# Optimization experiments

Hardware: AMD Instinct MI355X
Metric: run time of the kernel (lower is better)

Reference implementation:

```python
import jax, jax.numpy as jnp
import numpy as np

EMBED = 1024
HEADS = 16
HEAD_DIM = EMBED // HEADS


def setup_inputs() -> dict:
    key = jax.random.key(0)
    k1, k2, k3 = jax.random.split(key, 3)
    hidden_states = jax.random.normal(k1, (2, 2048, EMBED), dtype=jnp.float32)
    # Conv1D weights are stored (nx, nf): y = x @ W + b
    c_attn_w = jax.random.normal(k2, (EMBED, 3 * EMBED), dtype=jnp.float32) * 0.02
    c_attn_b = jnp.zeros((3 * EMBED,), dtype=jnp.float32)
    c_proj_w = jax.random.normal(k3, (EMBED, EMBED), dtype=jnp.float32) * 0.02
    c_proj_b = jnp.zeros((EMBED,), dtype=jnp.float32)
    return {
        "hidden_states": hidden_states,
        "c_attn_w": c_attn_w,
        "c_attn_b": c_attn_b,
        "c_proj_w": c_proj_w,
        "c_proj_b": c_proj_b,
    }


def reference(hidden_states, c_attn_w, c_attn_b, c_proj_w, c_proj_b):
    B, S, E = hidden_states.shape
    H, D = HEADS, HEAD_DIM
    fused = hidden_states @ c_attn_w + c_attn_b  # [B,S,3E]
    q, k, v = jnp.split(fused, 3, axis=-1)
    # split heads -> [B,H,S,D]
    q = q.reshape(B, S, H, D).transpose(0, 2, 1, 3)
    k = k.reshape(B, S, H, D).transpose(0, 2, 1, 3)
    v = v.reshape(B, S, H, D).transpose(0, 2, 1, 3)
    scores = jnp.einsum("bhqd,bhkd->bhqk", q, k) / jnp.sqrt(jnp.float32(D))
    probs = jax.nn.softmax(scores, axis=-1)  # NOTE: no causal mask in source
    attn = jnp.einsum("bhqk,bhkd->bhqd", probs, v)
    out = attn.transpose(0, 2, 1, 3).reshape(B, S, E)
    return out @ c_proj_w + c_proj_b
```

## Files before the change

### kernel.cpp

```cpp
#include <hip/hip_runtime.h>
#include <hip/hip_bf16.h>
#include <cstdint>
#include <cstddef>

#define E_ 1024
#define H_ 16
#define D_ 64
#define B_ 2
#define S_ 2048
#define T_ 4096
#define NQ_ 3072

typedef __bf16 bf16_t;
typedef bf16_t bf16x8 __attribute__((ext_vector_type(8)));
typedef float f32x4 __attribute__((ext_vector_type(4)));

static __device__ __forceinline__ unsigned short f2bf(float f) {
    __hip_bfloat16 h = __float2bfloat16(f);
    return __builtin_bit_cast(unsigned short, h);
}
static __device__ __forceinline__ unsigned pack2(float a, float b) {
    return (unsigned)f2bf(a) | ((unsigned)f2bf(b) << 16);
}
static __device__ __forceinline__ unsigned cvt_pk(float a, float b) {
    unsigned r;
    asm("v_cvt_pk_bf16_f32 %0, %1, %2" : "=v"(r) : "v"(a), "v"(b));
    return r;
}
static __device__ __forceinline__ bf16x8 ld_frag(const unsigned short* p) {
    uint4 u = *reinterpret_cast<const uint4*>(p);
    return __builtin_bit_cast(bf16x8, u);
}
static __device__ __forceinline__ void cp16(unsigned short* lds, const unsigned short* g) {
    __builtin_amdgcn_global_load_lds(
        (const __attribute__((address_space(1))) unsigned int*)g,
        (__attribute__((address_space(3))) unsigned int*)lds, 16, 0, 0);
}
static __device__ __forceinline__ f32x4 mfma16(bf16x8 a, bf16x8 b, f32x4 c) {
    return __builtin_amdgcn_mfma_f32_16x16x32_bf16(a, b, c, 0, 0, 0);
}

__global__ __launch_bounds__(256) void k_cvt(const float* __restrict__ in,
                                             unsigned short* __restrict__ out, int n) {
    int i = (blockIdx.x * 256 + threadIdx.x) * 4;
    if (i < n) {
        float4 v = *reinterpret_cast<const float4*>(in + i);
        uint2 o;
        o.x = pack2(v.x, v.y);
        o.y = pack2(v.z, v.w);
        *reinterpret_cast<uint2*>(out + i) = o;
    }
}

__global__ __launch_bounds__(256) void k_wt(const float* __restrict__ in,
                                            unsigned short* __restrict__ out, int K, int N) {
    __shared__ float t[32][33];
    int n0 = blockIdx.x * 32, k0 = blockIdx.y * 32;
    int tx = threadIdx.x, ty = threadIdx.y;
    for (int j = 0; j < 4; j++) {
        int r = ty + j * 8;
        t[r][tx] = in[(size_t)(k0 + r) * N + n0 + tx];
    }
    __syncthreads();
    for (int j = 0; j < 4; j++) {
        int r = ty + j * 8;
        out[(size_t)(n0 + r) * K + k0 + tx] = f2bf(t[tx][r]);
    }
}

static __device__ __forceinline__ void gemm_tile_128(
    const unsigned short* __restrict__ A,
    const unsigned short* __restrict__ Bt,
    int Ktot, int m0, int n0,
    unsigned short* As, unsigned short* Bs,
    f32x4 acc[4][4])
{
    const int t = threadIdx.x;
    const int w = t >> 6, lane = t & 63, lr = lane & 15, lq = lane >> 4;
    const int wm = (w >> 1) * 64, wn = (w & 1) * 64;
    for (int mt = 0; mt < 4; mt++)
        for (int nt = 0; nt < 4; nt++)
            acc[mt][nt] = (f32x4){0.f, 0.f, 0.f, 0.f};

    for (int kt = 0; kt < Ktot; kt += 32) {
        __syncthreads();
        for (int i = 0; i < 2; i++) {
            int c = t + i * 256;
            int row = c >> 2, kp = (c & 3) * 8;
            cp16(&As[c * 8], &A[(size_t)(m0 + row) * Ktot + kt + kp]);
        }
        for (int i = 0; i < 2; i++) {
            int c = t + i * 256;
            int row = c >> 2, kp = (c & 3) * 8;
            cp16(&Bs[c * 8], &Bt[(size_t)(n0 + row) * Ktot + kt + kp]);
        }
        __syncthreads();
        bf16x8 af[4], bfr[4];
        for (int mt = 0; mt < 4; mt++) af[mt]  = ld_frag(&As[(wm + mt * 16 + lr) * 32 + lq * 8]);
        for (int nt = 0; nt < 4; nt++) bfr[nt] = ld_frag(&Bs[(wn + nt * 16 + lr) * 32 + lq * 8]);
        for (int mt = 0; mt < 4; mt++)
            for (int nt = 0; nt < 4; nt++)
                acc[mt][nt] = mfma16(af[mt], bfr[nt], acc[mt][nt]);
    }
}

__global__ __launch_bounds__(256) void k_qkv(
    const unsigned short* __restrict__ Ab, const unsigned short* __restrict__ Wt,
    const float* __restrict__ bias,
    unsigned short* __restrict__ Qb, unsigned short* __restrict__ Kb,
    unsigned short* __restrict__ Vb)
{
    __shared__ __attribute__((aligned(16))) unsigned short As[128 * 32];
    __shared__ __attribute__((aligned(16))) unsigned short Bs[128 * 32];
    f32x4 acc[4][4];
    int m0 = blockIdx.x * 128, n0 = blockIdx.y * 128;
    gemm_tile_128(Ab, Wt, E_, m0, n0, As, Bs, acc);

    int t = threadIdx.x, w = t >> 6, lane = t & 63, lr = lane & 15, lq = lane >> 4;
    int wm = (w >> 1) * 64, wn = (w & 1) * 64;
    int sector = (n0 >> 10);
    for (int nt = 0; nt < 4; nt++) {
        int n = n0 + wn + nt * 16 + lr;
        float bv = bias[n];
        int nn = n & 1023, h = nn >> 6, d = nn & 63;
        for (int mt = 0; mt < 4; mt++) {
            for (int i = 0; i < 4; i++) {
                int tok = m0 + wm + mt * 16 + lq * 4 + i;
                int b = tok >> 11, s = tok & 2047;
                float v = acc[mt][nt][i] + bv;
                if (sector == 0) {
                    Qb[(((size_t)(b * H_ + h) * S_ + s) << 6) + d] = f2bf(v * 0.18033688f);
                } else if (sector == 1) {
                    Kb[(((size_t)(b * H_ + h) * S_ + s) << 6) + d] = f2bf(v);
                } else {
                    Vb[(((size_t)(b * H_ + h) * D_ + d) << 11) + s] = f2bf(v);
                }
            }
        }
    }
}

__global__ __launch_bounds__(256) void k_attn(
    const unsigned short* __restrict__ Qb, const unsigned short* __restrict__ Kb,
    const unsigned short* __restrict__ Vb, unsigned short* __restrict__ Ob)
{
    __shared__ __attribute__((aligned(16))) unsigned short Ks[2][128 * 64];
    __shared__ __attribute__((aligned(16))) unsigned short Vt[2][64 * 128];
    __shared__ __attribute__((aligned(16))) unsigned short Ps[4][32 * 64];

    const int t = threadIdx.x, w = t >> 6, lane = t & 63, lr = lane & 15, lq = lane >> 4;
    const int h = blockIdx.y, b = blockIdx.z;
    const size_t head = ((size_t)(b * H_ + h)) * (S_ * D_);
    const unsigned short* Qh = Qb + head;
    const unsigned short* Kh = Kb + head;
    const unsigned short* Vh = Vb + head;
    const int q0 = blockIdx.x * 128 + w * 16;
    const int swz = lr & 7;

    bf16x8 qa[2][2];
    for (int qh = 0; qh < 2; qh++)
        for (int kk = 0; kk < 2; kk++)
            qa[qh][kk] = ld_frag(&Qh[(size_t)(q0 + qh * 64 + lr) * 64 + kk * 32 + lq * 8]);

    f32x4 o[2][4];
    for (int qh = 0; qh < 2; qh++)
        for (int i = 0; i < 4; i++) o[qh][i] = (f32x4){0.f, 0.f, 0.f, 0.f};
    float lsum[2] = {0.f, 0.f};
    unsigned short* Pw = Ps[w];

    auto stage = [&](int bb, int kt) {
        for (int i = 0; i < 4; i++) {
            int c = t + i * 256;
            int row = c >> 3, sp = c & 7;
            cp16(&Ks[bb][c * 8], &Kh[(size_t)(kt + row) * 64 + (sp ^ (row & 7)) * 8]);
        }
        for (int i = 0; i < 4; i++) {
            int c = t + i * 256;
            int d = c >> 4, sp = c & 15, seg = (sp & 8) | ((sp & 7) ^ (d & 7));
            cp16(&Vt[bb][c * 8], &Vh[(size_t)d * S_ + kt + seg * 8]);
        }
    };

    stage(0, 0);
    asm volatile("s_waitcnt vmcnt(0)" ::: "memory");
    __syncthreads();

    int cur = 0;
#pragma unroll 2
    for (int kt = 0; kt < S_; kt += 128) {
        if (kt + 128 < S_) stage(cur ^ 1, kt + 128);

        const unsigned short* Kc = Ks[cur];
        const unsigned short* Vc = Vt[cur];

#pragma unroll
        for (int ss = 0; ss < 2; ss++) {
            for (int tau = 0; tau < 4; tau++) {
                int krow = ss * 64 + tau * 16 + lr;
                bf16x8 kf0 = ld_frag(&Kc[krow * 64 + ((0 + lq) ^ swz) * 8]);
                bf16x8 kf1 = ld_frag(&Kc[krow * 64 + ((4 + lq) ^ swz) * 8]);
                for (int qh = 0; qh < 2; qh++) {
                    f32x4 z = (f32x4){0.f, 0.f, 0.f, 0.f};
                    __builtin_amdgcn_s_setprio(1);
                    z = mfma16(kf0, qa[qh][0], z);
                    z = mfma16(kf1, qa[qh][1], z);
                    __builtin_amdgcn_s_setprio(0);
                    float e0 = __builtin_amdgcn_exp2f(z[0]);
                    float e1 = __builtin_amdgcn_exp2f(z[1]);
                    float e2 = __builtin_amdgcn_exp2f(z[2]);
                    float e3 = __builtin_amdgcn_exp2f(z[3]);
                    lsum[qh] += (e0 + e1) + (e2 + e3);
                    uint2 pk;
                    pk.x = cvt_pk(e0, e1);
                    pk.y = cvt_pk(e2, e3);
                    int seg = (tau * 2 + (lq >> 1)) ^ swz;
                    *reinterpret_cast<uint2*>(&Pw[(qh * 16 + lr) * 64 + seg * 8 + (lq & 1) * 4]) = pk;
                }
            }
            for (int kk = 0; kk < 2; kk++) {
                bf16x8 pf0 = ld_frag(&Pw[(lr) * 64 + ((kk * 4 + lq) ^ swz) * 8]);
                bf16x8 pf1 = ld_frag(&Pw[(16 + lr) * 64 + ((kk * 4 + lq) ^ swz) * 8]);
                __builtin_amdgcn_s_setprio(1);
                for (int t2 = 0; t2 < 4; t2++) {
                    int vrow = t2 * 16 + lr;
                    bf16x8 vf = ld_frag(&Vc[vrow * 128 + ((ss * 8) | ((kk * 4 + lq) ^ swz)) * 8]);
                    o[0][t2] = mfma16(vf, pf0, o[0][t2]);
                    o[1][t2] = mfma16(vf, pf1, o[1][t2]);
                }
                __builtin_amdgcn_s_setprio(0);
            }
        }

        asm volatile("s_waitcnt vmcnt(0)" ::: "memory");
        __syncthreads();
        cur ^= 1;
    }

    for (int qh = 0; qh < 2; qh++) {
        float ls = lsum[qh];
        ls += __shfl_xor(ls, 16, 64);
        ls += __shfl_xor(ls, 32, 64);
        float inv = 1.0f / ls;

        int s = q0 + qh * 64 + lr;
        size_t rowoff = ((size_t)(b * S_ + s)) * E_ + h * 64;
        for (int t2 = 0; t2 < 4; t2++) {
            uint2 pk;
            pk.x = cvt_pk(o[qh][t2][0] * inv, o[qh][t2][1] * inv);
            pk.y = cvt_pk(o[qh][t2][2] * inv, o[qh][t2][3] * inv);
            *reinterpret_cast<uint2*>(&Ob[rowoff + t2 * 16 + lq * 4]) = pk;
        }
    }
}

__global__ __launch_bounds__(256) void k_proj(
    const unsigned short* __restrict__ Ab, const unsigned short* __restrict__ Wt,
    const float* __restrict__ bias, float* __restrict__ out)
{
    __shared__ __attribute__((aligned(16))) unsigned short As[128 * 32];
    __shared__ __attribute__((aligned(16))) unsigned short Bs[64 * 32];
    const int t = threadIdx.x;
    const int w = t >> 6, lane = t & 63, lr = lane & 15, lq = lane >> 4;
    const int wm = (w >> 1) * 64, wn = (w & 1) * 32;
    const int m0 = blockIdx.x * 128, n0 = blockIdx.y * 64;

    f32x4 acc[4][2];
    for (int mt = 0; mt < 4; mt++)
        for (int nt = 0; nt < 2; nt++)
            acc[mt][nt] = (f32x4){0.f, 0.f, 0.f, 0.f};

    for (int kt = 0; kt < E_; kt += 32) {
        __syncthreads();
        for (int i = 0; i < 2; i++) {
            int c = t + i * 256;
            int row = c >> 2, kp = (c & 3) * 8;
            cp16(&As[c * 8], &Ab[(size_t)(m0 + row) * E_ + kt + kp]);
        }
        {
            int c = t;
            int row = c >> 2, kp = (c & 3) * 8;
            cp16(&Bs[c * 8], &Wt[(size_t)(n0 + row) * E_ + kt + kp]);
        }
        __syncthreads();
        bf16x8 af[4], bfr[2];
        for (int mt = 0; mt < 4; mt++) af[mt]  = ld_frag(&As[(wm + mt * 16 + lr) * 32 + lq * 8]);
        for (int nt = 0; nt < 2; nt++) bfr[nt] = ld_frag(&Bs[(wn + nt * 16 + lr) * 32 + lq * 8]);
        for (int mt = 0; mt < 4; mt++)
            for (int nt = 0; nt < 2; nt++)
                acc[mt][nt] = mfma16(af[mt], bfr[nt], acc[mt][nt]);
    }

    for (int nt = 0; nt < 2; nt++) {
        int n = n0 + wn + nt * 16 + lr;
        float bv = bias[n];
        for (int mt = 0; mt < 4; mt++)
            for (int i = 0; i < 4; i++) {
                int tok = m0 + wm + mt * 16 + lq * 4 + i;
                out[(size_t)tok * E_ + n] = acc[mt][nt][i] + bv;
            }
    }
}

extern "C" void kernel_launch(void* const* d_in, const int* in_sizes, int n_in,
                              void* d_out, int out_size, void* d_ws, size_t ws_size,
                              hipStream_t stream) {
    const float* hs = (const float*)d_in[0];
    const float* w1 = (const float*)d_in[1];
    const float* b1 = (const float*)d_in[2];
    const float* w2 = (const float*)d_in[3];
    const float* b2 = (const float*)d_in[4];
    float* out = (float*)d_out;

    char* ws = (char*)d_ws;
    unsigned short* hb  = (unsigned short*)(ws);
    unsigned short* w1t = (unsigned short*)(ws + (size_t)( 8 << 20));
    unsigned short* w2t = (unsigned short*)(ws + (size_t)(14 << 20));
    unsigned short* Qb  = (unsigned short*)(ws + (size_t)(16 << 20));
    unsigned short* Kb  = (unsigned short*)(ws + (size_t)(24 << 20));
    unsigned short* Vb  = (unsigned short*)(ws + (size_t)(32 << 20));
    unsigned short* Ao  = (unsigned short*)(ws + (size_t)(40 << 20));

    k_cvt<<<dim3(T_ * E_ / 1024), dim3(256), 0, stream>>>(hs, hb, T_ * E_);
    k_wt<<<dim3(NQ_ / 32, E_ / 32), dim3(32, 8), 0, stream>>>(w1, w1t, E_, NQ_);
    k_wt<<<dim3(E_ / 32, E_ / 32), dim3(32, 8), 0, stream>>>(w2, w2t, E_, E_);
    k_qkv<<<dim3(T_ / 128, NQ_ / 128), dim3(256), 0, stream>>>(hb, w1t, b1, Qb, Kb, Vb);
    k_attn<<<dim3(S_ / 128, H_, B_), dim3(256), 0, stream>>>(Qb, Kb, Vb, Ao);
    k_proj<<<dim3(T_ / 128, E_ / 64), dim3(256), 0, stream>>>(Ao, w2t, b2, out);
}
```

Baseline: 190.9 us.

## Double-buffer GEMM tiles in QKV and proj kernels, stage V transpose via LDS

Both the QKV and output-projection GEMMs now double-buffer their LDS tiles, issuing the next k-tile's global-to-LDS copies before computing on the current one, with one barrier per iteration instead of two. MFMA sections are wrapped in s_setprio to favour the math waves. The V output, stored transposed, is first staged in LDS so each thread writes contiguous 16-byte chunks instead of scattered 2-byte stores. This costs more shared memory per block, which may lower occupancy.

```diff
diff --git a/kernel.cpp b/kernel.cpp
--- a/kernel.cpp
+++ b/kernel.cpp
@@ -68,74 +68,105 @@
     }
 }
 
-static __device__ __forceinline__ void gemm_tile_128(
-    const unsigned short* __restrict__ A,
-    const unsigned short* __restrict__ Bt,
-    int Ktot, int m0, int n0,
-    unsigned short* As, unsigned short* Bs,
-    f32x4 acc[4][4])
-{
-    const int t = threadIdx.x;
-    const int w = t >> 6, lane = t & 63, lr = lane & 15, lq = lane >> 4;
-    const int wm = (w >> 1) * 64, wn = (w & 1) * 64;
-    for (int mt = 0; mt < 4; mt++)
-        for (int nt = 0; nt < 4; nt++)
-            acc[mt][nt] = (f32x4){0.f, 0.f, 0.f, 0.f};
-
-    for (int kt = 0; kt < Ktot; kt += 32) {
-        __syncthreads();
-        for (int i = 0; i < 2; i++) {
-            int c = t + i * 256;
-            int row = c >> 2, kp = (c & 3) * 8;
-            cp16(&As[c * 8], &A[(size_t)(m0 + row) * Ktot + kt + kp]);
-        }
-        for (int i = 0; i < 2; i++) {
-            int c = t + i * 256;
-            int row = c >> 2, kp = (c & 3) * 8;
-            cp16(&Bs[c * 8], &Bt[(size_t)(n0 + row) * Ktot + kt + kp]);
-        }
-        __syncthreads();
-        bf16x8 af[4], bfr[4];
-        for (int mt = 0; mt < 4; mt++) af[mt]  = ld_frag(&As[(wm + mt * 16 + lr) * 32 + lq * 8]);
-        for (int nt = 0; nt < 4; nt++) bfr[nt] = ld_frag(&Bs[(wn + nt * 16 + lr) * 32 + lq * 8]);
-        for (int mt = 0; mt < 4; mt++)
-            for (int nt = 0; nt < 4; nt++)
-                acc[mt][nt] = mfma16(af[mt], bfr[nt], acc[mt][nt]);
-    }
-}
-
 __global__ __launch_bounds__(256) void k_qkv(
     const unsigned short* __restrict__ Ab, const unsigned short* __restrict__ Wt,
     const float* __restrict__ bias,
     unsigned short* __restrict__ Qb, unsigned short* __restrict__ Kb,
     unsigned short* __restrict__ Vb)
 {
-    __shared__ __attribute__((aligned(16))) unsigned short As[128 * 32];
-    __shared__ __attribute__((aligned(16))) unsigned short Bs[128 * 32];
+    __shared__ __attribute__((aligned(16))) unsigned short smem[16896];
+    unsigned short* As = smem;
+    unsigned short* Bs = smem + 8192;
+
+    const int t = threadIdx.x;
+    const int w = t >> 6, lane = t & 63, lr = lane & 15, lq = lane >> 4;
+    const int wm = (w >> 1) * 64, wn = (w & 1) * 64;
+    const int m0 = blockIdx.x * 128, n0 = blockIdx.y * 128;
+
     f32x4 acc[4][4];
-    int m0 = blockIdx.x * 128, n0 = blockIdx.y * 128;
-    gemm_tile_128(Ab, Wt, E_, m0, n0, As, Bs, acc);
-
-    int t = threadIdx.x, w = t >> 6, lane = t & 63, lr = lane & 15, lq = lane >> 4;
-    int wm = (w >> 1) * 64, wn = (w & 1) * 64;
-    int sector = (n0 >> 10);
-    for (int nt = 0; nt < 4; nt++) {
-        int n = n0 + wn + nt * 16 + lr;
-        float bv = bias[n];
-        int nn = n & 1023, h = nn >> 6, d = nn & 63;
-        for (int mt = 0; mt < 4; mt++) {
-            for (int i = 0; i < 4; i++) {
-                int tok = m0 + wm + mt * 16 + lq * 4 + i;
-                int b = tok >> 11, s = tok & 2047;
-                float v = acc[mt][nt][i] + bv;
-                if (sector == 0) {
-                    Qb[(((size_t)(b * H_ + h) * S_ + s) << 6) + d] = f2bf(v * 0.18033688f);
-                } else if (sector == 1) {
-                    Kb[(((size_t)(b * H_ + h) * S_ + s) << 6) + d] = f2bf(v);
-                } else {
-                    Vb[(((size_t)(b * H_ + h) * D_ + d) << 11) + s] = f2bf(v);
+    for (int mt = 0; mt < 4; mt++)
+        for (int nt = 0; nt < 4; nt++)
+            acc[mt][nt] = (f32x4){0.f, 0.f, 0.f, 0.f};
+
+    auto stage = [&](int bb, int kt) {
+        for (int i = 0; i < 2; i++) {
+            int c = t + i * 256;
+            int row = c >> 2, kp = (c & 3) * 8;
+            cp16(&As[bb * 4096 + c * 8], &Ab[(size_t)(m0 + row) * E_ + kt + kp]);
+        }
+        for (int i = 0; i < 2; i++) {
+            int c = t + i * 256;
+            int row = c >> 2, kp = (c & 3) * 8;
+            cp16(&Bs[bb * 4096 + c * 8], &Wt[(size_t)(n0 + row) * E_ + kt + kp]);
+        }
+    };
+
+    stage(0, 0);
+    asm volatile("s_waitcnt vmcnt(0)" ::: "memory");
+    __syncthreads();
+
+    int cur = 0;
+    for (int kt = 0; kt < E_; kt += 32) {
+        if (kt + 32 < E_) stage(cur ^ 1, kt + 32);
+        const unsigned short* Ac = &As[cur * 4096];
+        const unsigned short* Bc = &Bs[cur * 4096];
+        bf16x8 af[4], bfr[4];
+        for (int mt = 0; mt < 4; mt++) af[mt]  = ld_frag(&Ac[(wm + mt * 16 + lr) * 32 + lq * 8]);
+        for (int nt = 0; nt < 4; nt++) bfr[nt] = ld_frag(&Bc[(wn + nt * 16 + lr) * 32 + lq * 8]);
+        __builtin_amdgcn_s_setprio(1);
+        for (int mt = 0; mt < 4; mt++)
+            for (int nt = 0; nt < 4; nt++)
+                acc[mt][nt] = mfma16(af[mt], bfr[nt], acc[mt][nt]);
+        __builtin_amdgcn_s_setprio(0);
+        asm volatile("s_waitcnt vmcnt(0)" ::: "memory");
+        __syncthreads();
+        cur ^= 1;
+    }
+
+    const int sector = (n0 >> 10);
+    if (sector != 2) {
+        for (int nt = 0; nt < 4; nt++) {
+            int n = n0 + wn + nt * 16 + lr;
+            float bv = bias[n];
+            int nn = n & 1023, h = nn >> 6, d = nn & 63;
+            for (int mt = 0; mt < 4; mt++) {
+                for (int i = 0; i < 4; i++) {
+                    int tok = m0 + wm + mt * 16 + lq * 4 + i;
+                    int b = tok >> 11, s = tok & 2047;
+                    float v = acc[mt][nt][i] + bv;
+                    if (sector == 0) {
+                        Qb[(((size_t)(b * H_ + h) * S_ + s) << 6) + d] = f2bf(v * 0.18033688f);
+                    } else {
+                        Kb[(((size_t)(b * H_ + h) * S_ + s) << 6) + d] = f2bf(v);
+                    }
                 }
             }
+        }
+    } else {
+        for (int nt = 0; nt < 4; nt++) {
+            int nl = wn + nt * 16 + lr;
+            int row = nl;
+            float bv = bias[n0 + nl];
+            unsigned short* vr = &smem[row * 132];
+            for (int mt = 0; mt < 4; mt++) {
+                int tokb = wm + mt * 16 + lq * 4;
+                uint2 pk;
+                pk.x = cvt_pk(acc[mt][nt][0] + bv, acc[mt][nt][1] + bv);
+                pk.y = cvt_pk(acc[mt][nt][2] + bv, acc[mt][nt][3] + bv);
+                *reinterpret_cast<uint2*>(&vr[tokb]) = pk;
+            }
+        }
+        __syncthreads();
+        int row = t >> 1, half = t & 1;
+        int hglob = ((n0 & 1023) >> 6) + (row >> 6), d = row & 63;
+        int b = m0 >> 11, sbase = (m0 & 2047) + half * 64;
+        size_t gb = (((size_t)(b * H_ + hglob) * D_ + d) << 11) + sbase;
+        const unsigned short* src = &smem[row * 132 + half * 64];
+        for (int jj = 0; jj < 8; jj++) {
+            uint2 a = *reinterpret_cast<const uint2*>(&src[jj * 8]);
+            uint2 bq = *reinterpret_cast<const uint2*>(&src[jj * 8 + 4]);
+            uint4 o4; o4.x = a.x; o4.y = a.y; o4.z = bq.x; o4.w = bq.y;
+            *reinterpret_cast<uint4*>(&Vb[gb + jj * 8]) = o4;
         }
     }
 }
@@ -257,8 +288,10 @@
     const unsigned short* __restrict__ Ab, const unsigned short* __restrict__ Wt,
     const float* __restrict__ bias, float* __restrict__ out)
 {
-    __shared__ __attribute__((aligned(16))) unsigned short As[128 * 32];
-    __shared__ __attribute__((aligned(16))) unsigned short Bs[64 * 32];
+    __shared__ __attribute__((aligned(16))) unsigned short smem[12288];
+    unsigned short* As = smem;
+    unsigned short* Bs = smem + 8192;
+
     const int t = threadIdx.x;
     const int w = t >> 6, lane = t & 63, lr = lane & 15, lq = lane >> 4;
     const int wm = (w >> 1) * 64, wn = (w & 1) * 32;
@@ -269,25 +302,39 @@
         for (int nt = 0; nt < 2; nt++)
             acc[mt][nt] = (f32x4){0.f, 0.f, 0.f, 0.f};
 
-    for (int kt = 0; kt < E_; kt += 32) {
-        __syncthreads();
+    auto stage = [&](int bb, int kt) {
         for (int i = 0; i < 2; i++) {
             int c = t + i * 256;
             int row = c >> 2, kp = (c & 3) * 8;
-            cp16(&As[c * 8], &Ab[(size_t)(m0 + row) * E_ + kt + kp]);
+            cp16(&As[bb * 4096 + c * 8], &Ab[(size_t)(m0 + row) * E_ + kt + kp]);
         }
         {
             int c = t;
             int row = c >> 2, kp = (c & 3) * 8;
-            cp16(&Bs[c * 8], &Wt[(size_t)(n0 + row) * E_ + kt + kp]);
-        }
-        __syncthreads();
+            cp16(&Bs[bb * 2048 + c * 8], &Wt[(size_t)(n0 + row) * E_ + kt + kp]);
+        }
+    };
+
+    stage(0, 0);
+    asm volatile("s_waitcnt vmcnt(0)" ::: "memory");
+    __syncthreads();
+
+    int cur = 0;
+    for (int kt = 0; kt < E_; kt += 32) {
+        if (kt + 32 < E_) stage(cur ^ 1, kt + 32);
+        const unsigned short* Ac = &As[cur * 4096];
+        const unsigned short* Bc = &Bs[cur * 2048];
         bf16x8 af[4], bfr[2];
-        for (int mt = 0; mt < 4; mt++) af[mt]  = ld_frag(&As[(wm + mt * 16 + lr) * 32 + lq * 8]);
-        for (int nt = 0; nt < 2; nt++) bfr[nt] = ld_frag(&Bs[(wn + nt * 16 + lr) * 32 + lq * 8]);
+        for (int mt = 0; mt < 4; mt++) af[mt]  = ld_frag(&Ac[(wm + mt * 16 + lr) * 32 + lq * 8]);
+        for (int nt = 0; nt < 2; nt++) bfr[nt] = ld_frag(&Bc[(wn + nt * 16 + lr) * 32 + lq * 8]);
+        __builtin_amdgcn_s_setprio(1);
         for (int mt = 0; mt < 4; mt++)
             for (int nt = 0; nt < 2; nt++)
                 acc[mt][nt] = mfma16(af[mt], bfr[nt], acc[mt][nt]);
+        __builtin_amdgcn_s_setprio(0);
+        asm volatile("s_waitcnt vmcnt(0)" ::: "memory");
+        __syncthreads();
+        cur ^= 1;
     }
 
     for (int nt = 0; nt < 2; nt++) {
```

Result: slower. 202.5 us (+6.1%).
